# Kernel tuning notes

Measured on AMD Instinct MI355X. Metric: run time of the kernel, lower is better.

The kernel has to match this reference:

```python
import jax, jax.numpy as jnp
import numpy as np

N = 50000        # nodes per type (MiRNA=0, Disease=1, LncRNA=2)
E = 500000       # edges per relation
F_IN, HID, OUT = 128, 64, 64
ITEMS, SIZE, T = 4096, 4096, 100
# relation order: MvsD, DvsM, MvsL, LvsM, LvsD, DvsL
SRC = (0, 1, 0, 2, 2, 1)
DST = (1, 0, 2, 0, 1, 2)


def _sage_hetero_layer(h, edges, Wp, bp, Ws, bs, Wn):
    """One HeteroGraphConv(SAGEConv pool, aggregate='sum') layer.
    h: list of 3 [N, Fin] node-feature arrays; edges: [6, 2, E] int."""
    n = h[0].shape[0]
    out = [None, None, None]
    for e in range(6):
        s, d = SRC[e], DST[e]
        pooled = jax.nn.relu(h[s] @ Wp[e] + bp[e])                 # [N, Fin]
        msg = pooled[edges[e, 0]]                                  # [E, Fin] gather at src
        agg = jax.ops.segment_max(msg, edges[e, 1], num_segments=n)
        agg = jnp.where(jnp.isneginf(agg), 0.0, agg)               # DGL: 0 for isolated dst
        o = h[d] @ Ws[e] + bs[e] + agg @ Wn[e]                     # fc_self(+bias) + fc_neigh
        out[d] = o if out[d] is None else out[d] + o
    return out


def setup_inputs() -> dict:
    key = jax.random.key(0)
    ks = jax.random.split(key, 32)
    s = 0.05
    inp = {
        'hM': jax.random.normal(ks[0], (N, F_IN), jnp.float32),
        'hD': jax.random.normal(ks[1], (N, F_IN), jnp.float32),
        'hL': jax.random.normal(ks[2], (N, F_IN), jnp.float32),
        'Wpool1': jax.random.normal(ks[3], (6, F_IN, F_IN), jnp.float32) * s,
        'bpool1': jnp.zeros((6, F_IN), jnp.float32),
        'Wself1': jax.random.normal(ks[4], (6, F_IN, HID), jnp.float32) * s,
        'bself1': jnp.zeros((6, HID), jnp.float32),
        'Wneigh1': jax.random.normal(ks[5], (6, F_IN, HID), jnp.float32) * s,
        'Wpool2': jax.random.normal(ks[6], (6, HID, HID), jnp.float32) * s,
        'bpool2': jnp.zeros((6, HID), jnp.float32),
        'Wself2': jax.random.normal(ks[7], (6, HID, HID), jnp.float32) * s,
        'bself2': jnp.zeros((6, HID), jnp.float32),
        'Wneigh2': jax.random.normal(ks[8], (6, HID, HID), jnp.float32) * s,
        'Wpool3': jax.random.normal(ks[9], (6, HID, HID), jnp.float32) * s,
        'bpool3': jnp.zeros((6, HID), jnp.float32),
        'Wself3': jax.random.normal(ks[10], (6, HID, OUT), jnp.float32) * s,
        'bself3': jnp.zeros((6, OUT), jnp.float32),
        'Wneigh3': jax.random.normal(ks[11], (6, HID, OUT), jnp.float32) * s,
        'Adj': jax.random.uniform(ks[12], (SIZE, ITEMS), jnp.float32),
        'noise': jax.random.normal(ks[13], (N, OUT), jnp.float32),
        'W1': jax.random.normal(ks[14], (ITEMS + OUT, 256), jnp.float32) * s,
        'b1': jnp.zeros((256,), jnp.float32),
        'W2': jax.random.normal(ks[15], (256, 512), jnp.float32) * s,
        'b2': jnp.zeros((512,), jnp.float32),
        'W3': jax.random.normal(ks[16], (512, 1024), jnp.float32) * s,
        'b3': jnp.zeros((1024,), jnp.float32),
        'W4': jax.random.normal(ks[17], (1024, ITEMS), jnp.float32) * s,
        'b4': jnp.zeros((ITEMS,), jnp.float32),
        'edges': jax.random.randint(ks[18], (6, 2, E), 0, N, jnp.int32),
        't': 50,
        'size': SIZE,
        'leftIndex': 0,
    }
    return inp


def reference(hM, hD, hL, Wpool1, bpool1, Wself1, bself1, Wneigh1,
              Wpool2, bpool2, Wself2, bself2, Wneigh2,
              Wpool3, bpool3, Wself3, bself3, Wneigh3,
              Adj, noise, W1, b1, W2, b2, W3, b3, W4, b4,
              edges, t, size, leftIndex):
    h1 = _sage_hetero_layer([hM, hD, hL], edges, Wpool1, bpool1, Wself1, bself1, Wneigh1)
    h2 = _sage_hetero_layer(h1, edges, Wpool2, bpool2, Wself2, bself2, Wneigh2)
    h3 = _sage_hetero_layer(h2, edges, Wpool3, bpool3, Wself3, bself3, Wneigh3)
    mirna = h3[0]                                                  # [N, OUT]
    mirna = mirna / jnp.maximum(jnp.sum(jnp.abs(mirna), axis=1, keepdims=True), 1e-12)
    # diffusion schedule
    betas = jnp.linspace(1e-4, 0.02, T, dtype=jnp.float32)
    alpha_bars = jnp.cumprod(1.0 - betas)
    signal_rates = jnp.sqrt(alpha_bars)
    noise_rates = jnp.sqrt(1.0 - alpha_bars)
    noisy = signal_rates[t] * mirna + noise_rates[t] * noise
    fake = jax.lax.stop_gradient(noisy[leftIndex:leftIndex + size])  # detach + slice
    M = jnp.concatenate([Adj, fake], axis=1)                       # [size, ITEMS+OUT]
    x = jax.nn.relu(M @ W1 + b1)
    x = jax.nn.relu(x @ W2 + b2)
    x = jax.nn.relu(x @ W3 + b3)
    x = jax.nn.sigmoid(x @ W4 + b4)
    return fake, x
```

## Files before the change

kernel.cpp:

```cpp
#include <hip/hip_runtime.h>
#include <hip/hip_bf16.h>

#define NNODE 50000
#define NEDGE 500000
#define SZ    4096
#define NBKT  256
#define BWID  196
#define BCAP  4096
#define RELEB ((size_t)NBKT * BCAP)
#define ZK1   13

typedef __attribute__((ext_vector_type(8))) short bf16x8;
typedef __attribute__((ext_vector_type(4))) float f32x4;

__device__ __forceinline__ float bits2f(unsigned short u) {
    return __uint_as_float(((unsigned)u) << 16);
}
__device__ __forceinline__ unsigned short f2bits(float f) {
    unsigned x = __float_as_uint(f);
    unsigned r = x + 0x7fffu + ((x >> 16) & 1u);
    return (unsigned short)(r >> 16);
}
__device__ __forceinline__ unsigned pk_max_u16(unsigned a, unsigned b) {
    unsigned lo = max(a & 0xffffu, b & 0xffffu);
    unsigned hi = max(a >> 16, b >> 16);
    return lo | (hi << 16);
}
__device__ __forceinline__ void gl_lds16(const void* g, void* l) {
    __builtin_amdgcn_global_load_lds(
        (const __attribute__((address_space(1))) unsigned int*)g,
        (__attribute__((address_space(3))) unsigned int*)l, 16, 0, 0);
}

template<int RELU, int SIG, int OUTF32, int PART>
__global__ __launch_bounds__(256)
void gemm128(const unsigned short* __restrict__ A, const unsigned short* __restrict__ Bt,
             const float* __restrict__ bias, void* __restrict__ Cv, int M, int N, int K)
{
    __shared__ unsigned short As[128 * 64];
    __shared__ unsigned short Bs[128 * 64];
    const int tid = threadIdx.x;
    const int wave = tid >> 6, lane = tid & 63;
    const int m16 = lane & 15, quad = lane >> 4;
    const int wr = wave >> 1, wc = wave & 1;
    const int nwg = gridDim.x * gridDim.y;
    int bid = blockIdx.y * gridDim.x + blockIdx.x;
    if ((nwg & 7) == 0) { int cpx = nwg >> 3; bid = (bid & 7) * cpx + (bid >> 3); }
    const int bx = bid % gridDim.x, by = bid / gridDim.x;
    const int row0 = by * 128, col0 = bx * 128;
    const int lrow = lane >> 3, lcol = (lane & 7) * 8;

    f32x4 acc[4][4] = {};

    int k0beg = 0, k0end = K;
    if (PART) {
        const int per = ((K >> 6) + gridDim.z - 1) / gridDim.z;
        k0beg = blockIdx.z * per * 64;
        k0end = min(K, k0beg + per * 64);
    }

    for (int k0 = k0beg; k0 < k0end; k0 += 64) {
#pragma unroll
        for (int i = 0; i < 4; ++i) {
            int chunk = wave * 4 + i;
            int row = chunk * 8 + lrow;
            gl_lds16(A  + (size_t)(row0 + row) * K + k0 + lcol, &As[chunk * 512]);
            gl_lds16(Bt + (size_t)(col0 + row) * K + k0 + lcol, &Bs[chunk * 512]);
        }
        __syncthreads();
#pragma unroll
        for (int ks = 0; ks < 2; ++ks) {
            bf16x8 a[4], b[4];
#pragma unroll
            for (int mt = 0; mt < 4; ++mt)
                a[mt] = *(const bf16x8*)&As[(wr * 64 + mt * 16 + m16) * 64 + ks * 32 + quad * 8];
#pragma unroll
            for (int nt = 0; nt < 4; ++nt)
                b[nt] = *(const bf16x8*)&Bs[(wc * 64 + nt * 16 + m16) * 64 + ks * 32 + quad * 8];
#pragma unroll
            for (int mt = 0; mt < 4; ++mt)
#pragma unroll
                for (int nt = 0; nt < 4; ++nt)
                    acc[mt][nt] = __builtin_amdgcn_mfma_f32_16x16x32_bf16(a[mt], b[nt], acc[mt][nt], 0, 0, 0);
        }
        __syncthreads();
    }

    if (PART) {
        float* P = (float*)Cv + (size_t)blockIdx.z * M * N;
#pragma unroll
        for (int mt = 0; mt < 4; ++mt)
#pragma unroll
            for (int nt = 0; nt < 4; ++nt) {
                int gc = col0 + wc * 64 + nt * 16 + m16;
#pragma unroll
                for (int r = 0; r < 4; ++r) {
                    int gm = row0 + wr * 64 + mt * 16 + quad * 4 + r;
                    P[(size_t)gm * N + gc] = acc[mt][nt][r];
                }
            }
        return;
    }

#pragma unroll
    for (int mt = 0; mt < 4; ++mt) {
#pragma unroll
        for (int nt = 0; nt < 4; ++nt) {
            int gc = col0 + wc * 64 + nt * 16 + m16;
            float bv = bias[gc];
#pragma unroll
            for (int r = 0; r < 4; ++r) {
                int gm = row0 + wr * 64 + mt * 16 + quad * 4 + r;
                size_t idx = (size_t)gm * N + gc;
                float v = acc[mt][nt][r] + bv;
                if (RELU) v = fmaxf(v, 0.f);
                if (SIG)  v = 1.f / (1.f + __expf(-v));
                if (OUTF32) ((float*)Cv)[idx] = v;
                else        ((unsigned short*)Cv)[idx] = f2bits(v);
            }
        }
    }
}

__global__ __launch_bounds__(256)
void mlp1_ep_k(const float* __restrict__ p, const float* __restrict__ b1,
               unsigned short* __restrict__ x1)
{
    const size_t MN = (size_t)SZ * 256;
    int i = blockIdx.x * 256 + threadIdx.x;
    if (i >= (int)(MN / 4)) return;
    float4 s = ((const float4*)p)[i];
#pragma unroll
    for (int z = 1; z < ZK1; ++z) {
        float4 a = ((const float4*)(p + (size_t)z * MN))[i];
        s.x += a.x; s.y += a.y; s.z += a.z; s.w += a.w;
    }
    int base = i * 4;
    ushort4 o;
    o.x = f2bits(fmaxf(s.x + b1[(base + 0) & 255], 0.f));
    o.y = f2bits(fmaxf(s.y + b1[(base + 1) & 255], 0.f));
    o.z = f2bits(fmaxf(s.z + b1[(base + 2) & 255], 0.f));
    o.w = f2bits(fmaxf(s.w + b1[(base + 3) & 255], 0.f));
    ((ushort4*)x1)[i] = o;
}

template<int NT>
__global__ __launch_bounds__(256)
void pool2_k(const unsigned short* __restrict__ A0, const unsigned short* __restrict__ A1,
             const unsigned short* __restrict__ Bt0, const unsigned short* __restrict__ Bt1,
             const float* __restrict__ b0, const float* __restrict__ b1,
             unsigned short* __restrict__ out, int M, int K)
{
    __shared__ unsigned short As[64][72];
    __shared__ unsigned short Bs[NT * 16][72];
    const int z = blockIdx.z;
    const unsigned short* A = z ? A1 : A0;
    const unsigned short* Bt = z ? Bt1 : Bt0;
    const float* bias = z ? b1 : b0;
    const int N = NT * 16;
    unsigned short* Cv = out + (size_t)z * M * N;

    const int tid = threadIdx.x;
    const int wave = tid >> 6, lane = tid & 63;
    const int m16 = lane & 15, quad = lane >> 4;
    const int row0 = blockIdx.y * 64, col0 = blockIdx.x * N;

    f32x4 acc[NT] = {};

    for (int k0 = 0; k0 < K; k0 += 64) {
#pragma unroll
        for (int it = 0; it < 2; ++it) {
            int u = tid + it * 256;
            int m = u >> 3, c = (u & 7) * 8;
            int gm = row0 + m;
            uint4 v = make_uint4(0u, 0u, 0u, 0u);
            if (gm < M) v = *(const uint4*)(A + (size_t)gm * K + k0 + c);
            *(uint4*)&As[m][c] = v;
        }
#pragma unroll
        for (int it = 0; it < NT / 2; ++it) {
            int u = tid + it * 256;
            int n = u >> 3, c = (u & 7) * 8;
            uint4 v = *(const uint4*)(Bt + (size_t)(col0 + n) * K + k0 + c);
            *(uint4*)&Bs[n][c] = v;
        }
        __syncthreads();
#pragma unroll
        for (int ks = 0; ks < 2; ++ks) {
            bf16x8 a = *(const bf16x8*)&As[wave * 16 + m16][ks * 32 + quad * 8];
#pragma unroll
            for (int nt = 0; nt < NT; ++nt) {
                bf16x8 b = *(const bf16x8*)&Bs[nt * 16 + m16][ks * 32 + quad * 8];
                acc[nt] = __builtin_amdgcn_mfma_f32_16x16x32_bf16(a, b, acc[nt], 0, 0, 0);
            }
        }
        __syncthreads();
    }

#pragma unroll
    for (int nt = 0; nt < NT; ++nt) {
        int gc = col0 + nt * 16 + m16;
        float bv = bias[gc];
#pragma unroll
        for (int r = 0; r < 4; ++r) {
            int gm = row0 + wave * 16 + quad * 4 + r;
            if (gm < M)
                Cv[(size_t)gm * N + gc] = f2bits(fmaxf(acc[nt][r] + bv, 0.f));
        }
    }
}

template<int NT>
__global__ __launch_bounds__(256)
void mfma_gemm(const unsigned short* __restrict__ A1, const unsigned short* __restrict__ A2,
               const unsigned short* __restrict__ A3,
               const unsigned short* __restrict__ Bt, const float* __restrict__ bias,
               const float* __restrict__ bias2,
               unsigned short* __restrict__ Cv, int M, int N, int Ka, int Kb, int Kc)
{
    __shared__ unsigned short As[64][72];
    __shared__ unsigned short Bs[NT * 16][72];
    const int tid = threadIdx.x;
    const int wave = tid >> 6, lane = tid & 63;
    const int m16 = lane & 15, quad = lane >> 4;
    const int row0 = blockIdx.y * 64, col0 = blockIdx.x * (NT * 16);
    const int K = Ka + Kb + Kc;

    f32x4 acc[NT] = {};

    for (int k0 = 0; k0 < K; k0 += 64) {
        const int seg = (k0 >= Ka + Kb) ? 2 : ((k0 >= Ka) ? 1 : 0);
        const unsigned short* src = seg == 2 ? A3 : (seg == 1 ? A2 : A1);
        const int ld = seg == 2 ? Kc : (seg == 1 ? Kb : Ka);
        const int kb = k0 - (seg == 2 ? Ka + Kb : (seg == 1 ? Ka : 0));
#pragma unroll
        for (int it = 0; it < 2; ++it) {
            int u = tid + it * 256;
            int m = u >> 3, c = (u & 7) * 8;
            int gm = row0 + m;
            uint4 v = make_uint4(0u, 0u, 0u, 0u);
            if (gm < M) v = *(const uint4*)(src + (size_t)gm * ld + kb + c);
            *(uint4*)&As[m][c] = v;
        }
#pragma unroll
        for (int it = 0; it < NT / 2; ++it) {
            int u = tid + it * 256;
            int n = u >> 3, c = (u & 7) * 8;
            uint4 v = *(const uint4*)(Bt + (size_t)(col0 + n) * K + k0 + c);
            *(uint4*)&Bs[n][c] = v;
        }
        __syncthreads();
#pragma unroll
        for (int ks = 0; ks < 2; ++ks) {
            bf16x8 a = *(const bf16x8*)&As[wave * 16 + m16][ks * 32 + quad * 8];
#pragma unroll
            for (int nt = 0; nt < NT; ++nt) {
                bf16x8 b = *(const bf16x8*)&Bs[nt * 16 + m16][ks * 32 + quad * 8];
                acc[nt] = __builtin_amdgcn_mfma_f32_16x16x32_bf16(a, b, acc[nt], 0, 0, 0);
            }
        }
        __syncthreads();
    }

#pragma unroll
    for (int nt = 0; nt < NT; ++nt) {
        int gc = col0 + nt * 16 + m16;
        float bv = bias[gc] + bias2[gc];
#pragma unroll
        for (int r = 0; r < 4; ++r) {
            int gm = row0 + wave * 16 + quad * 4 + r;
            if (gm < M)
                Cv[(size_t)gm * N + gc] = f2bits(acc[nt][r] + bv);
        }
    }
}

__global__ __launch_bounds__(256)
void transpose_cvt(const float* __restrict__ src1, const float* __restrict__ src2,
                   unsigned short* __restrict__ dst, int R1, int R2, int Nn)
{
    __shared__ float tile[32][33];
    const int R = R1 + R2;
    const int e = blockIdx.z;
    src1 += (size_t)e * R1 * Nn;
    if (src2) src2 += (size_t)e * R2 * Nn;
    dst += (size_t)e * Nn * R;
    const int r0 = blockIdx.x * 32, n0 = blockIdx.y * 32;
    const int lr = threadIdx.x >> 5, ln = threadIdx.x & 31;
#pragma unroll
    for (int i = 0; i < 4; ++i) {
        int r = r0 + lr + i * 8, n = n0 + ln;
        float v = 0.f;
        if (r < R && n < Nn) v = (r < R1) ? src1[(size_t)r * Nn + n]
                                          : src2[(size_t)(r - R1) * Nn + n];
        tile[lr + i * 8][ln] = v;
    }
    __syncthreads();
#pragma unroll
    for (int i = 0; i < 4; ++i) {
        int n = n0 + lr + i * 8, r = r0 + ln;
        if (n < Nn && r < R) dst[(size_t)n * R + r] = f2bits(tile[ln][lr + i * 8]);
    }
}

__global__ __launch_bounds__(256)
void fuse_w_k(const float* __restrict__ Ws, const float* __restrict__ Wn,
              unsigned short* __restrict__ dst, int F)
{
    const int PAe[3] = {1, 0, 2}, PBe[3] = {3, 4, 5};
    __shared__ float tile[32][33];
    const int p = blockIdx.z;
    const int eA = PAe[p], eB = PBe[p];
    const int Kt = 3 * F;
    unsigned short* D = dst + (size_t)p * 64 * Kt;
    const int r0 = blockIdx.x * 32;
    const int n0 = blockIdx.y * 32;
    const int lr = threadIdx.x >> 5, ln = threadIdx.x & 31;
    for (int seg = 0; seg < 3; ++seg) {
        __syncthreads();
#pragma unroll
        for (int i = 0; i < 4; ++i) {
            int r = r0 + lr + i * 8, n = n0 + ln;
            float v;
            if (seg == 0)
                v = Ws[((size_t)eA * F + r) * 64 + n] + Ws[((size_t)eB * F + r) * 64 + n];
            else if (seg == 1)
                v = Wn[((size_t)eA * F + r) * 64 + n];
            else
                v = Wn[((size_t)eB * F + r) * 64 + n];
            tile[lr + i * 8][ln] = v;
        }
        __syncthreads();
        const int koff = seg * F;
#pragma unroll
        for (int i = 0; i < 4; ++i) {
            int n = n0 + lr + i * 8, r = r0 + ln;
            D[(size_t)n * Kt + koff + r] = f2bits(tile[ln][lr + i * 8]);
        }
    }
}

__global__ __launch_bounds__(256)
void cvt3_k(const float* __restrict__ s0, const float* __restrict__ s1,
            const float* __restrict__ s2, unsigned short* __restrict__ dst)
{
    const int z = blockIdx.z;
    const float* src = z == 0 ? s0 : (z == 1 ? s1 : s2);
    dst += (size_t)z * NNODE * 128;
    int i = blockIdx.x * 256 + threadIdx.x;
    if (i >= 1600000) return;
    float4 v = ((const float4*)src)[i];
    ushort4 w;
    w.x = f2bits(v.x); w.y = f2bits(v.y); w.z = f2bits(v.z); w.w = f2bits(v.w);
    ((ushort4*)dst)[i] = w;
}

__global__ __launch_bounds__(256)
void cvt_adj_k(const float* __restrict__ src, unsigned short* __restrict__ dst)
{
    int i = blockIdx.x * 256 + threadIdx.x;
    if (i >= 4194304) return;
    int r = i >> 10, c4 = i & 1023;
    float4 v = ((const float4*)src)[i];
    ushort4 w;
    w.x = f2bits(v.x); w.y = f2bits(v.y); w.z = f2bits(v.z); w.w = f2bits(v.w);
    *(ushort4*)(dst + (size_t)r * 4160 + c4 * 4) = w;
}

__global__ __launch_bounds__(256)
void binit_k(int* __restrict__ bcur)
{
    bcur[blockIdx.x * NBKT + threadIdx.x] = threadIdx.x * BCAP;
}

__global__ __launch_bounds__(256)
void bucket_k(const int* __restrict__ edges, int* __restrict__ bcur,
              unsigned* __restrict__ ebuf)
{
    const int r = blockIdx.y;
    const int base = blockIdx.x * 4096;
    const int tid = threadIdx.x;
    __shared__ int lcnt[NBKT];
    __shared__ int lbase[NBKT];
    for (int i = tid; i < NBKT; i += 256) lcnt[i] = 0;
    __syncthreads();
    unsigned ent[16];
    int rnk[16];
#pragma unroll
    for (int i = 0; i < 16; ++i) {
        int e = base + tid + i * 256;
        ent[i] = 0xffffffffu;
        rnk[i] = 0;
        if (e < NEDGE) {
            int src = edges[(size_t)r * 2 * NEDGE + e];
            int dst = edges[(size_t)r * 2 * NEDGE + NEDGE + e];
            ent[i] = ((unsigned)dst << 16) | (unsigned)src;
            rnk[i] = atomicAdd(&lcnt[dst / BWID], 1);
        }
    }
    __syncthreads();
    for (int i = tid; i < NBKT; i += 256)
        lbase[i] = lcnt[i] ? atomicAdd(&bcur[r * NBKT + i], lcnt[i]) : 0;
    __syncthreads();
#pragma unroll
    for (int i = 0; i < 16; ++i)
        if (ent[i] != 0xffffffffu) {
            int b = (int)(ent[i] >> 16) / BWID;
            int pos = lbase[b] + rnk[i];
            if (pos < (b + 1) * BCAP)
                ebuf[(size_t)r * RELEB + pos] = ent[i];
        }
}

__global__ __launch_bounds__(256)
void bscan_k(const int* __restrict__ bcur, int* __restrict__ bbase,
             int* __restrict__ offs)
{
    const int r = blockIdx.x, tid = threadIdx.x;
    const int lane = tid & 63, wv = tid >> 6;
    int v = bcur[r * NBKT + tid] - tid * BCAP;
    if (v > BCAP) v = BCAP;
    int x = v;
#pragma unroll
    for (int off = 1; off < 64; off <<= 1) {
        int t = __shfl_up(x, off);
        if (lane >= off) x += t;
    }
    __shared__ int wsum[4];
    if (lane == 63) wsum[wv] = x;
    __syncthreads();
    int add = 0;
#pragma unroll
    for (int w = 0; w < 4; ++w) if (w < wv) add += wsum[w];
    x += add;
    bbase[r * NBKT + tid] = x - v;
    if (tid == 255) offs[(size_t)r * (NNODE + 1) + NNODE] = x;
}

__global__ __launch_bounds__(256)
void debucket_k(const unsigned* __restrict__ ebuf, const int* __restrict__ bcur,
                const int* __restrict__ bbase, int* __restrict__ offs,
                unsigned short* __restrict__ srcs)
{
    const int r = blockIdx.y, b = blockIdx.x, tid = threadIdx.x;
    const int lo = b * BWID;
    __shared__ unsigned es[BCAP];
    __shared__ unsigned short stage[BCAP];
    __shared__ int lhist[256];
    __shared__ int buf[256];
    __shared__ int lcur[256];
    int cnt = bcur[r * NBKT + b] - b * BCAP;
    if (cnt > BCAP) cnt = BCAP;
    const int base = bbase[r * NBKT + b];
    lhist[tid] = 0;
    __syncthreads();
    for (int j = tid; j < cnt; j += 256) {
        unsigned e = ebuf[(size_t)r * RELEB + (size_t)b * BCAP + j];
        es[j] = e;
        atomicAdd(&lhist[(int)(e >> 16) - lo], 1);
    }
    __syncthreads();
    int v = lhist[tid];
    buf[tid] = v;
    __syncthreads();
    for (int off = 1; off < 256; off <<= 1) {
        int t = (tid >= off) ? buf[tid - off] : 0;
        __syncthreads();
        buf[tid] += t;
        __syncthreads();
    }
    int excl = buf[tid] - v;
    int node = lo + tid;
    if (tid < BWID && node < NNODE) offs[(size_t)r * (NNODE + 1) + node] = base + excl;
    lcur[tid] = excl;
    __syncthreads();
    for (int j = tid; j < cnt; j += 256) {
        unsigned e = es[j];
        int d = (int)(e >> 16) - lo;
        int p = atomicAdd(&lcur[d], 1);
        stage[p] = (unsigned short)(e & 0xffffu);
    }
    __syncthreads();
    for (int j = tid; j < cnt; j += 256)
        srcs[(size_t)r * NEDGE + base + j] = stage[j];
}

template<int F>
__global__ __launch_bounds__(256)
void gather2_k(const unsigned short* __restrict__ pooled, const int* __restrict__ offs,
               const unsigned short* __restrict__ srcs, unsigned short* __restrict__ agg,
               int e0, int e1)
{
    const int CG = F / 8;
    const int z = blockIdx.z;
    const int e = z ? e1 : e0;
    pooled += (size_t)z * NNODE * F;
    agg    += (size_t)z * NNODE * F;
    offs   += (size_t)e * (NNODE + 1);
    srcs   += (size_t)e * NEDGE;
    int idx = blockIdx.x * 256 + threadIdx.x;
    int n = idx / CG, cg = idx % CG;
    if (n >= NNODE) return;
    int beg = offs[n], end = offs[n + 1];
    unsigned m0 = 0, m1 = 0, m2 = 0, m3 = 0;
    int j = beg;
    for (; j + 4 <= end; j += 4) {
        int s0 = srcs[j], s1 = srcs[j + 1], s2 = srcs[j + 2], s3 = srcs[j + 3];
        uint4 v0 = *(const uint4*)(pooled + (size_t)s0 * F + cg * 8);
        uint4 v1 = *(const uint4*)(pooled + (size_t)s1 * F + cg * 8);
        uint4 v2 = *(const uint4*)(pooled + (size_t)s2 * F + cg * 8);
        uint4 v3 = *(const uint4*)(pooled + (size_t)s3 * F + cg * 8);
        m0 = pk_max_u16(m0, pk_max_u16(pk_max_u16(v0.x, v1.x), pk_max_u16(v2.x, v3.x)));
        m1 = pk_max_u16(m1, pk_max_u16(pk_max_u16(v0.y, v1.y), pk_max_u16(v2.y, v3.y)));
        m2 = pk_max_u16(m2, pk_max_u16(pk_max_u16(v0.z, v1.z), pk_max_u16(v2.z, v3.z)));
        m3 = pk_max_u16(m3, pk_max_u16(pk_max_u16(v0.w, v1.w), pk_max_u16(v2.w, v3.w)));
    }
    for (; j < end; ++j) {
        int s = srcs[j];
        uint4 v = *(const uint4*)(pooled + (size_t)s * F + cg * 8);
        m0 = pk_max_u16(m0, v.x);
        m1 = pk_max_u16(m1, v.y);
        m2 = pk_max_u16(m2, v.z);
        m3 = pk_max_u16(m3, v.w);
    }
    uint4 o; o.x = m0; o.y = m1; o.z = m2; o.w = m3;
    *(uint4*)(agg + (size_t)n * F + cg * 8) = o;
}

__global__ __launch_bounds__(64)
void fake_k(const unsigned short* __restrict__ mirna, const float* __restrict__ noise,
            const int* __restrict__ t_p, const int* __restrict__ left_p,
            unsigned short* __restrict__ adj_s, float* __restrict__ fake_out)
{
    int r = blockIdx.x, c = threadIdx.x;
    int t = *t_p, left = *left_p;
    int row = left + r;
    float x = bits2f(mirna[(size_t)row * 64 + c]);
    float s = fabsf(x);
#pragma unroll
    for (int off = 32; off > 0; off >>= 1) s += __shfl_down(s, off);
    s = __shfl(s, 0);
    float ab = 1.f;
    for (int i = 0; i <= t; ++i)
        ab *= (1.f - (1e-4f + (0.02f - 1e-4f) * ((float)i / 99.f)));
    float v = sqrtf(ab) * (x / fmaxf(s, 1e-12f)) + sqrtf(1.f - ab) * noise[(size_t)row * 64 + c];
    adj_s[(size_t)r * 4160 + 4096 + c] = f2bits(v);
    fake_out[(size_t)r * 64 + c] = v;
}

extern "C" void kernel_launch(void* const* d_in, const int* in_sizes, int n_in,
                              void* d_out, int out_size, void* d_ws, size_t ws_size,
                              hipStream_t stream)
{
    const float* h0[3]    = {(const float*)d_in[0], (const float*)d_in[1], (const float*)d_in[2]};
    const float* Wpool[3] = {(const float*)d_in[3], (const float*)d_in[8],  (const float*)d_in[13]};
    const float* bpool[3] = {(const float*)d_in[4], (const float*)d_in[9],  (const float*)d_in[14]};
    const float* bself[3] = {(const float*)d_in[6], (const float*)d_in[11], (const float*)d_in[16]};
    const float* Wself[3] = {(const float*)d_in[5], (const float*)d_in[10], (const float*)d_in[15]};
    const float* Wneigh[3]= {(const float*)d_in[7], (const float*)d_in[12], (const float*)d_in[17]};
    const float* Adj   = (const float*)d_in[18];
    const float* noise = (const float*)d_in[19];
    const float* W1 = (const float*)d_in[20]; const float* b1 = (const float*)d_in[21];
    const float* W2 = (const float*)d_in[22]; const float* b2 = (const float*)d_in[23];
    const float* W3 = (const float*)d_in[24]; const float* b3 = (const float*)d_in[25];
    const float* W4 = (const float*)d_in[26]; const float* b4 = (const float*)d_in[27];
    const int* edges  = (const int*)d_in[28];
    const int* t_p    = (const int*)d_in[29];
    const int* left_p = (const int*)d_in[31];

    unsigned short* ws = (unsigned short*)d_ws;
    const size_t P1 = 0, P2 = 98304, P3 = 122880;
    const size_t FU1 = 147456, FU2 = 245760, FU3 = 294912;
    const size_t W1T = 344064, W2T = 1409024, W3T = 1540096, W4T = 2064384;
    const size_t ADJ = 6258688;
    const size_t POOLED = 23298048;
    const size_t AGGB = 29698048;
    const size_t HA = 36098048, HB = 45698048;
    int* bcur  = (int*)(ws + 55298048);
    int* bbase = bcur + 6 * NBKT;
    int* offs  = bbase + 6 * NBKT;
    unsigned short* srcs = (unsigned short*)(offs + 6 * (NNODE + 1));
    unsigned* ebuf = (unsigned*)(ws + POOLED);
    unsigned short* x1 = ws + POOLED;
    unsigned short* x2 = x1 + (size_t)SZ * 256;
    unsigned short* x3 = x2 + (size_t)SZ * 512;
    unsigned short* adj_s = ws + ADJ;
    float* out_fake = (float*)d_out;
    float* out_x    = out_fake + (size_t)SZ * 64;
    unsigned short* hb0 = (unsigned short*)out_x;
    unsigned short* agg2_l1 = hb0 + 19200000;
    float* x1p = out_x;

    const int SRCr[6] = {0, 1, 0, 2, 2, 1};
    const int PAe[3] = {1, 0, 2}, PBe[3] = {3, 4, 5};
    dim3 T(256);

    transpose_cvt<<<dim3(4, 4, 6),   T, 0, stream>>>(Wpool[0], nullptr, ws + P1, 128, 0, 128);
    transpose_cvt<<<dim3(2, 2, 6),   T, 0, stream>>>(Wpool[1], nullptr, ws + P2, 64, 0, 64);
    transpose_cvt<<<dim3(2, 2, 6),   T, 0, stream>>>(Wpool[2], nullptr, ws + P3, 64, 0, 64);
    fuse_w_k<<<dim3(4, 2, 3), T, 0, stream>>>(Wself[0], Wneigh[0], ws + FU1, 128);
    fuse_w_k<<<dim3(2, 2, 3), T, 0, stream>>>(Wself[1], Wneigh[1], ws + FU2, 64);
    fuse_w_k<<<dim3(2, 2, 3), T, 0, stream>>>(Wself[2], Wneigh[2], ws + FU3, 64);
    transpose_cvt<<<dim3(130, 8, 1), T, 0, stream>>>(W1, nullptr, ws + W1T, 4160, 0, 256);
    transpose_cvt<<<dim3(8, 16, 1),  T, 0, stream>>>(W2, nullptr, ws + W2T, 256, 0, 512);
    transpose_cvt<<<dim3(16, 32, 1), T, 0, stream>>>(W3, nullptr, ws + W3T, 512, 0, 1024);
    transpose_cvt<<<dim3(32, 128, 1),T, 0, stream>>>(W4, nullptr, ws + W4T, 1024, 0, 4096);
    cvt_adj_k<<<16384, T, 0, stream>>>(Adj, adj_s);
    cvt3_k<<<dim3(6250, 1, 3), T, 0, stream>>>(h0[0], h0[1], h0[2], hb0);

    binit_k<<<6, T, 0, stream>>>(bcur);
    bucket_k<<<dim3(123, 6), T, 0, stream>>>(edges, bcur, ebuf);
    bscan_k<<<6, T, 0, stream>>>(bcur, bbase, offs);
    debucket_k<<<dim3(NBKT, 6), T, 0, stream>>>(ebuf, bcur, bbase, offs, srcs);

    for (int p = 0; p < 3; ++p) {
        const int eA = PAe[p], eB = PBe[p];
        pool2_k<8><<<dim3(1, 782, 2), T, 0, stream>>>(
            hb0 + (size_t)SRCr[eA] * NNODE * 128, hb0 + (size_t)SRCr[eB] * NNODE * 128,
            ws + P1 + (size_t)eA * 16384, ws + P1 + (size_t)eB * 16384,
            bpool[0] + eA * 128, bpool[0] + eB * 128,
            ws + POOLED, NNODE, 128);
        gather2_k<128><<<dim3(3125, 1, 2), T, 0, stream>>>(
            ws + POOLED, offs, srcs, agg2_l1, eA, eB);
        mfma_gemm<4><<<dim3(1, 782), T, 0, stream>>>(
            hb0 + (size_t)p * NNODE * 128, agg2_l1, agg2_l1 + (size_t)NNODE * 128,
            ws + FU1 + (size_t)p * 24576, bself[0] + eA * 64, bself[0] + eB * 64,
            ws + HA + (size_t)p * NNODE * 64, NNODE, 64, 128, 128, 128);
    }

    unsigned short* hin = ws + HA;
    unsigned short* hout = ws + HB;
    for (int layer = 1; layer <= 2; ++layer) {
        const unsigned short* pT = ws + (layer == 1 ? P2 : P3);
        const unsigned short* fT = ws + (layer == 1 ? FU2 : FU3);
        const float* bp = bpool[layer];
        const float* bs_ = bself[layer];
        for (int p = 0; p < 3; ++p) {
            const int eA = PAe[p], eB = PBe[p];
            pool2_k<4><<<dim3(1, 782, 2), T, 0, stream>>>(
                hin + (size_t)SRCr[eA] * NNODE * 64, hin + (size_t)SRCr[eB] * NNODE * 64,
                pT + (size_t)eA * 4096, pT + (size_t)eB * 4096,
                bp + eA * 64, bp + eB * 64,
                ws + POOLED, NNODE, 64);
            gather2_k<64><<<dim3(1563, 1, 2), T, 0, stream>>>(
                ws + POOLED, offs, srcs, ws + AGGB, eA, eB);
            mfma_gemm<4><<<dim3(1, 782), T, 0, stream>>>(
                hin + (size_t)p * NNODE * 64, ws + AGGB, ws + AGGB + (size_t)NNODE * 64,
                fT + (size_t)p * 12288, bs_ + eA * 64, bs_ + eB * 64,
                hout + (size_t)p * NNODE * 64, NNODE, 64, 64, 64, 64);
        }
        unsigned short* tmp = hin; hin = hout; hout = tmp;
    }

    fake_k<<<SZ, dim3(64), 0, stream>>>(hin, noise, t_p, left_p, adj_s, out_fake);

    gemm128<0, 0, 0, 1><<<dim3(2, 32, ZK1), T, 0, stream>>>(
        adj_s, ws + W1T, b1, x1p, SZ, 256, 4160);
    mlp1_ep_k<<<1024, T, 0, stream>>>(x1p, b1, x1);
    gemm128<1, 0, 0, 0><<<dim3(4, 32),  T, 0, stream>>>(x1, ws + W2T, b2, x2, SZ, 512, 256);
    gemm128<1, 0, 0, 0><<<dim3(8, 32),  T, 0, stream>>>(x2, ws + W3T, b3, x3, SZ, 1024, 512);
    gemm128<0, 1, 1, 0><<<dim3(32, 32), T, 0, stream>>>(x3, ws + W4T, b4, out_x, SZ, 4096, 1024);
}
```

Before: 961.7 us.

## Batch all six relations per layer into single pool, gather, and GEMM launches

For layers 2 and 3, the per-pair loop of three pool/gather/GEMM launch triples is replaced by one launch each that covers all six relations (or all three destination types) through blockIdx.z. The aim is fewer kernel launches and more concurrent blocks per launch, so the GPU is better filled and the serialized gaps between small kernels go away. The cost is larger intermediate buffers: pooled and aggregated outputs for all relations live at once, split across the output buffer and workspace, which raises memory footprint and the risk of aliasing with other live data.

```diff
diff --git a/kernel.cpp b/kernel.cpp
--- a/kernel.cpp
+++ b/kernel.cpp
@@ -210,6 +210,69 @@
     }
 }
 
+__global__ __launch_bounds__(256)
+void pool6_k(const unsigned short* __restrict__ hin, const unsigned short* __restrict__ pT,
+             const float* __restrict__ bp, unsigned short* __restrict__ pooled6, int M)
+{
+    const int SRCr[6] = {0, 1, 0, 2, 2, 1};
+    __shared__ unsigned short As[64][72];
+    __shared__ unsigned short Bs[64][72];
+    const int z = blockIdx.z;
+    const unsigned short* A = hin + (size_t)SRCr[z] * M * 64;
+    const unsigned short* Bt = pT + (size_t)z * 4096;
+    const float* bias = bp + z * 64;
+    unsigned short* Cv = pooled6 + (size_t)z * M * 64;
+
+    const int tid = threadIdx.x;
+    const int wave = tid >> 6, lane = tid & 63;
+    const int m16 = lane & 15, quad = lane >> 4;
+    const int row0 = blockIdx.y * 64;
+
+    f32x4 acc[4] = {};
+
+    {
+        const int k0 = 0;
+#pragma unroll
+        for (int it = 0; it < 2; ++it) {
+            int u = tid + it * 256;
+            int m = u >> 3, c = (u & 7) * 8;
+            int gm = row0 + m;
+            uint4 v = make_uint4(0u, 0u, 0u, 0u);
+            if (gm < M) v = *(const uint4*)(A + (size_t)gm * 64 + k0 + c);
+            *(uint4*)&As[m][c] = v;
+        }
+#pragma unroll
+        for (int it = 0; it < 2; ++it) {
+            int u = tid + it * 256;
+            int n = u >> 3, c = (u & 7) * 8;
+            uint4 v = *(const uint4*)(Bt + (size_t)n * 64 + k0 + c);
+            *(uint4*)&Bs[n][c] = v;
+        }
+        __syncthreads();
+#pragma unroll
+        for (int ks = 0; ks < 2; ++ks) {
+            bf16x8 a = *(const bf16x8*)&As[wave * 16 + m16][ks * 32 + quad * 8];
+#pragma unroll
+            for (int nt = 0; nt < 4; ++nt) {
+                bf16x8 b = *(const bf16x8*)&Bs[nt * 16 + m16][ks * 32 + quad * 8];
+                acc[nt] = __builtin_amdgcn_mfma_f32_16x16x32_bf16(a, b, acc[nt], 0, 0, 0);
+            }
+        }
+    }
+
+#pragma unroll
+    for (int nt = 0; nt < 4; ++nt) {
+        int gc = nt * 16 + m16;
+        float bv = bias[gc];
+#pragma unroll
+        for (int r = 0; r < 4; ++r) {
+            int gm = row0 + wave * 16 + quad * 4 + r;
+            if (gm < M)
+                Cv[(size_t)gm * 64 + gc] = f2bits(fmaxf(acc[nt][r] + bv, 0.f));
+        }
+    }
+}
+
 template<int NT>
 __global__ __launch_bounds__(256)
 void mfma_gemm(const unsigned short* __restrict__ A1, const unsigned short* __restrict__ A2,
@@ -271,6 +334,78 @@
             int gm = row0 + wave * 16 + quad * 4 + r;
             if (gm < M)
                 Cv[(size_t)gm * N + gc] = f2bits(acc[nt][r] + bv);
+        }
+    }
+}
+
+__global__ __launch_bounds__(256)
+void fused3_k(const unsigned short* __restrict__ hin,
+              const unsigned short* __restrict__ regA, const unsigned short* __restrict__ regB,
+              const unsigned short* __restrict__ fT, const float* __restrict__ bs,
+              unsigned short* __restrict__ hout, int M)
+{
+    const int PAe[3] = {1, 0, 2}, PBe[3] = {3, 4, 5};
+    __shared__ unsigned short As[64][72];
+    __shared__ unsigned short Bs[64][72];
+    const int z = blockIdx.z;
+    const int eA = PAe[z], eB = PBe[z];
+    const unsigned short* A1 = hin + (size_t)z * M * 64;
+    const unsigned short* A2 = (eA < 4) ? regA + (size_t)eA * M * 64 : regB + (size_t)(eA - 4) * M * 64;
+    const unsigned short* A3 = (eB < 4) ? regA + (size_t)eB * M * 64 : regB + (size_t)(eB - 4) * M * 64;
+    const unsigned short* Bt = fT + (size_t)z * 12288;
+    const float* bias = bs + eA * 64;
+    const float* bias2 = bs + eB * 64;
+    unsigned short* Cv = hout + (size_t)z * M * 64;
+
+    const int tid = threadIdx.x;
+    const int wave = tid >> 6, lane = tid & 63;
+    const int m16 = lane & 15, quad = lane >> 4;
+    const int row0 = blockIdx.y * 64;
+
+    f32x4 acc[4] = {};
+
+#pragma unroll
+    for (int seg = 0; seg < 3; ++seg) {
+        const unsigned short* src = seg == 2 ? A3 : (seg == 1 ? A2 : A1);
+        const int k0 = seg * 64;
+#pragma unroll
+        for (int it = 0; it < 2; ++it) {
+            int u = tid + it * 256;
+            int m = u >> 3, c = (u & 7) * 8;
+            int gm = row0 + m;
+            uint4 v = make_uint4(0u, 0u, 0u, 0u);
+            if (gm < M) v = *(const uint4*)(src + (size_t)gm * 64 + c);
+            *(uint4*)&As[m][c] = v;
+        }
+#pragma unroll
+        for (int it = 0; it < 2; ++it) {
+            int u = tid + it * 256;
+            int n = u >> 3, c = (u & 7) * 8;
+            uint4 v = *(const uint4*)(Bt + (size_t)n * 192 + k0 + c);
+            *(uint4*)&Bs[n][c] = v;
+        }
+        __syncthreads();
+#pragma unroll
+        for (int ks = 0; ks < 2; ++ks) {
+            bf16x8 a = *(const bf16x8*)&As[wave * 16 + m16][ks * 32 + quad * 8];
+#pragma unroll
+            for (int nt = 0; nt < 4; ++nt) {
+                bf16x8 b = *(const bf16x8*)&Bs[nt * 16 + m16][ks * 32 + quad * 8];
+                acc[nt] = __builtin_amdgcn_mfma_f32_16x16x32_bf16(a, b, acc[nt], 0, 0, 0);
+            }
+        }
+        __syncthreads();
+    }
+
+#pragma unroll
+    for (int nt = 0; nt < 4; ++nt) {
+        int gc = nt * 16 + m16;
+        float bv = bias[gc] + bias2[gc];
+#pragma unroll
+        for (int r = 0; r < 4; ++r) {
+            int gm = row0 + wave * 16 + quad * 4 + r;
+            if (gm < M)
+                Cv[(size_t)gm * 64 + gc] = f2bits(acc[nt][r] + bv);
         }
     }
 }
@@ -527,6 +662,47 @@
     *(uint4*)(agg + (size_t)n * F + cg * 8) = o;
 }
 
+__global__ __launch_bounds__(256)
+void gather6_k(const unsigned short* __restrict__ pooled6, const int* __restrict__ offs,
+               const unsigned short* __restrict__ srcs,
+               unsigned short* __restrict__ regA, unsigned short* __restrict__ regB)
+{
+    const int F = 64, CG = 8;
+    const int z = blockIdx.z;
+    const unsigned short* pooled = pooled6 + (size_t)z * NNODE * F;
+    unsigned short* agg = (z < 4) ? regA + (size_t)z * NNODE * F
+                                  : regB + (size_t)(z - 4) * NNODE * F;
+    offs += (size_t)z * (NNODE + 1);
+    srcs += (size_t)z * NEDGE;
+    int idx = blockIdx.x * 256 + threadIdx.x;
+    int n = idx / CG, cg = idx % CG;
+    if (n >= NNODE) return;
+    int beg = offs[n], end = offs[n + 1];
+    unsigned m0 = 0, m1 = 0, m2 = 0, m3 = 0;
+    int j = beg;
+    for (; j + 4 <= end; j += 4) {
+        int s0 = srcs[j], s1 = srcs[j + 1], s2 = srcs[j + 2], s3 = srcs[j + 3];
+        uint4 v0 = *(const uint4*)(pooled + (size_t)s0 * F + cg * 8);
+        uint4 v1 = *(const uint4*)(pooled + (size_t)s1 * F + cg * 8);
+        uint4 v2 = *(const uint4*)(pooled + (size_t)s2 * F + cg * 8);
+        uint4 v3 = *(const uint4*)(pooled + (size_t)s3 * F + cg * 8);
+        m0 = pk_max_u16(m0, pk_max_u16(pk_max_u16(v0.x, v1.x), pk_max_u16(v2.x, v3.x)));
+        m1 = pk_max_u16(m1, pk_max_u16(pk_max_u16(v0.y, v1.y), pk_max_u16(v2.y, v3.y)));
+        m2 = pk_max_u16(m2, pk_max_u16(pk_max_u16(v0.z, v1.z), pk_max_u16(v2.z, v3.z)));
+        m3 = pk_max_u16(m3, pk_max_u16(pk_max_u16(v0.w, v1.w), pk_max_u16(v2.w, v3.w)));
+    }
+    for (; j < end; ++j) {
+        int s = srcs[j];
+        uint4 v = *(const uint4*)(pooled + (size_t)s * F + cg * 8);
+        m0 = pk_max_u16(m0, v.x);
+        m1 = pk_max_u16(m1, v.y);
+        m2 = pk_max_u16(m2, v.z);
+        m3 = pk_max_u16(m3, v.w);
+    }
+    uint4 o; o.x = m0; o.y = m1; o.z = m2; o.w = m3;
+    *(uint4*)(agg + (size_t)n * F + cg * 8) = o;
+}
+
 __global__ __launch_bounds__(64)
 void fake_k(const unsigned short* __restrict__ mirna, const float* __restrict__ noise,
             const int* __restrict__ t_p, const int* __restrict__ left_p,
@@ -574,7 +750,6 @@
     const size_t W1T = 344064, W2T = 1409024, W3T = 1540096, W4T = 2064384;
     const size_t ADJ = 6258688;
     const size_t POOLED = 23298048;
-    const size_t AGGB = 29698048;
     const size_t HA = 36098048, HB = 45698048;
     int* bcur  = (int*)(ws + 55298048);
     int* bbase = bcur + 6 * NBKT;
@@ -589,6 +764,9 @@
     float* out_x    = out_fake + (size_t)SZ * 64;
     unsigned short* hb0 = (unsigned short*)out_x;
     unsigned short* agg2_l1 = hb0 + 19200000;
+    unsigned short* pooled6 = (unsigned short*)out_x;
+    unsigned short* aggB6 = pooled6 + 19200000;
+    unsigned short* aggA6 = ws + POOLED;
     float* x1p = out_x;
 
     const int SRCr[6] = {0, 1, 0, 2, 2, 1};
@@ -633,22 +811,10 @@
     for (int layer = 1; layer <= 2; ++layer) {
         const unsigned short* pT = ws + (layer == 1 ? P2 : P3);
         const unsigned short* fT = ws + (layer == 1 ? FU2 : FU3);
-        const float* bp = bpool[layer];
-        const float* bs_ = bself[layer];
-        for (int p = 0; p < 3; ++p) {
-            const int eA = PAe[p], eB = PBe[p];
-            pool2_k<4><<<dim3(1, 782, 2), T, 0, stream>>>(
-                hin + (size_t)SRCr[eA] * NNODE * 64, hin + (size_t)SRCr[eB] * NNODE * 64,
-                pT + (size_t)eA * 4096, pT + (size_t)eB * 4096,
-                bp + eA * 64, bp + eB * 64,
-                ws + POOLED, NNODE, 64);
-            gather2_k<64><<<dim3(1563, 1, 2), T, 0, stream>>>(
-                ws + POOLED, offs, srcs, ws + AGGB, eA, eB);
-            mfma_gemm<4><<<dim3(1, 782), T, 0, stream>>>(
-                hin + (size_t)p * NNODE * 64, ws + AGGB, ws + AGGB + (size_t)NNODE * 64,
-                fT + (size_t)p * 12288, bs_ + eA * 64, bs_ + eB * 64,
-                hout + (size_t)p * NNODE * 64, NNODE, 64, 64, 64, 64);
-        }
+        pool6_k<<<dim3(1, 782, 6), T, 0, stream>>>(hin, pT, bpool[layer], pooled6, NNODE);
+        gather6_k<<<dim3(1563, 1, 6), T, 0, stream>>>(pooled6, offs, srcs, aggA6, aggB6);
+        fused3_k<<<dim3(1, 782, 3), T, 0, stream>>>(hin, aggA6, aggB6, fT,
+                                                    bself[layer], hout, NNODE);
         unsigned short* tmp = hin; hin = hout; hout = tmp;
     }
 
```

New measurement: 891.8 us. 1.08x faster.
